# Performance work log

Hardware: AMD Instinct MI355X
Metric: run time of the kernel (lower is better)

Reference implementation:

```python
import jax, jax.numpy as jnp
import numpy as np

N = 100000
F_IN = 256
F_OUT = 64
E = 3200000
NEG_SLOPE = 0.2


def setup_inputs() -> dict:
    key = jax.random.key(0)
    k1, k2, k3, k4, k5 = jax.random.split(key, 5)
    x = jax.random.normal(k1, (N, F_IN), dtype=jnp.float32)
    edge_index = jax.random.randint(k2, (2, E), 0, N, dtype=jnp.int32)
    # GATConv params (heads=1): lin weight, att_src, att_dst, bias
    W = jax.random.normal(k3, (F_IN, F_OUT), dtype=jnp.float32) / np.sqrt(F_IN)
    att_src = jax.random.normal(k4, (F_OUT,), dtype=jnp.float32) / np.sqrt(F_OUT)
    att_dst = jax.random.normal(k5, (F_OUT,), dtype=jnp.float32) / np.sqrt(F_OUT)
    bias = jnp.zeros((F_OUT,), dtype=jnp.float32)
    return {"x": x, "edge_index": edge_index, "W": W,
            "att_src": att_src, "att_dst": att_dst, "bias": bias}


def reference(x, edge_index, W, att_src, att_dst, bias):
    n = x.shape[0]
    h = x @ W  # [N, F_OUT]
    # add self-loops (PyG default add_self_loops=True)
    loops = jnp.arange(n, dtype=edge_index.dtype)
    src = jnp.concatenate([edge_index[0], loops])  # message source j
    dst = jnp.concatenate([edge_index[1], loops])  # message target i
    # per-node attention halves
    a_src = h @ att_src  # [N]
    a_dst = h @ att_dst  # [N]
    e = a_src[src] + a_dst[dst]  # [E+N]
    e = jnp.where(e > 0, e, NEG_SLOPE * e)  # LeakyReLU(0.2)
    # softmax over edges grouped by target node
    e_max = jax.ops.segment_max(e, dst, num_segments=n)
    e_max = jnp.where(jnp.isfinite(e_max), e_max, 0.0)
    p = jnp.exp(e - e_max[dst])
    denom = jax.ops.segment_sum(p, dst, num_segments=n)
    alpha = p / (denom[dst] + 1e-16)  # [E+N]
    # scatter-aggregate weighted source features
    out = jax.ops.segment_sum(alpha[:, None] * h[src], dst, num_segments=n)
    return out + bias
```

## Files before the change

kernel.cpp:

```cpp
#include <hip/hip_runtime.h>
#include <hip/hip_bf16.h>
#include <math.h>

#define F_IN 256
#define F_OUT 64
#define NEG_SLOPE 0.2f
#define SHIFT 7
#define NPB 128
#define MAXK 1024
#define CAP 4608
#define OVF 4
#define GRID_B 256

__device__ __forceinline__ float bf2f(__hip_bfloat16 v) {
    return __bfloat162float(v);
}

typedef short short8 __attribute__((ext_vector_type(8)));
typedef float f32x4 __attribute__((ext_vector_type(4)));

__device__ __forceinline__ unsigned int bf16_bits(float v) {
    unsigned int u = __float_as_uint(v);
    return (u + 0x7fffu + ((u >> 16) & 1u)) >> 16;
}

#define WHI(q, c, l) (((((q)*4 + (c)) * 64) + (l)) * 8)
#define WLO(q, c, l) (16384 + WHI(q, c, l))

__global__ __launch_bounds__(512, 2) void gemm_kernel(
    const float* __restrict__ x, const float* __restrict__ W,
    const float* __restrict__ att_src, const float* __restrict__ att_dst,
    __hip_bfloat16* __restrict__ h16, float* __restrict__ a_src,
    float* __restrict__ a_dst, int N, int nTiles)
{
    __shared__ unsigned short sW[32768];

    const int t = threadIdx.x;
    const int lane = t & 63;
    const int w = t >> 6;
    const int g = lane >> 4;
    const int fr = lane & 15;

    for (int idx = t; idx < 2048; idx += 512) {
        const int q = idx >> 8;
        const int c = (idx >> 6) & 3;
        const int l = idx & 63;
        const int col = c * 16 + (l & 15);
        const float* wp = W + (size_t)(q * 32 + ((l >> 4) * 8)) * F_OUT + col;
        short8 hv, lv;
#pragma unroll
        for (int e = 0; e < 8; e++) {
            float wv = wp[(size_t)e * F_OUT];
            unsigned int hb = bf16_bits(wv);
            float hf = __uint_as_float(hb << 16);
            unsigned int lb = bf16_bits(wv - hf);
            hv[e] = (short)hb;
            lv[e] = (short)lb;
        }
        *(short8*)&sW[WHI(q, c, l)] = hv;
        *(short8*)&sW[WLO(q, c, l)] = lv;
    }
    __syncthreads();

    float as4[4], ad4[4];
#pragma unroll
    for (int c = 0; c < 4; c++) {
        as4[c] = att_src[c * 16 + fr];
        ad4[c] = att_dst[c * 16 + fr];
    }

    const float4 z4 = make_float4(0.f, 0.f, 0.f, 0.f);

    for (int tile = blockIdx.x; tile < nTiles; tile += gridDim.x) {
        const int R0 = tile * 128 + w * 16;
        const int rowA = R0 + fr;
        const bool okA = rowA < N;
        const float* xrow = x + (size_t)rowA * F_IN + g * 8;

        f32x4 acc[4];
#pragma unroll
        for (int c = 0; c < 4; c++) acc[c] = (f32x4){0.f, 0.f, 0.f, 0.f};

        float4 cur0 = okA ? *(const float4*)(xrow + 0) : z4;
        float4 cur1 = okA ? *(const float4*)(xrow + 4) : z4;

#pragma unroll
        for (int q = 0; q < 8; q++) {
            float4 nxt0 = z4, nxt1 = z4;
            if (q < 7) {
                nxt0 = okA ? *(const float4*)(xrow + (q + 1) * 32)     : z4;
                nxt1 = okA ? *(const float4*)(xrow + (q + 1) * 32 + 4) : z4;
            }

            const float vf[8] = {cur0.x, cur0.y, cur0.z, cur0.w,
                                 cur1.x, cur1.y, cur1.z, cur1.w};
            short8 ahi, alo;
#pragma unroll
            for (int e = 0; e < 8; e++) {
                unsigned int hb = bf16_bits(vf[e]);
                float hf = __uint_as_float(hb << 16);
                unsigned int lb = bf16_bits(vf[e] - hf);
                ahi[e] = (short)hb;
                alo[e] = (short)lb;
            }
#pragma unroll
            for (int c = 0; c < 4; c++) {
                short8 bh = *(const short8*)&sW[WHI(q, c, lane)];
                short8 bl = *(const short8*)&sW[WLO(q, c, lane)];
                acc[c] = __builtin_amdgcn_mfma_f32_16x16x32_bf16(ahi, bh, acc[c], 0, 0, 0);
                acc[c] = __builtin_amdgcn_mfma_f32_16x16x32_bf16(alo, bh, acc[c], 0, 0, 0);
                acc[c] = __builtin_amdgcn_mfma_f32_16x16x32_bf16(ahi, bl, acc[c], 0, 0, 0);
            }
            cur0 = nxt0;
            cur1 = nxt1;
            __builtin_amdgcn_sched_barrier(0);
        }

        float sr[4] = {0.f, 0.f, 0.f, 0.f};
        float sd[4] = {0.f, 0.f, 0.f, 0.f};
#pragma unroll
        for (int c = 0; c < 4; c++) {
#pragma unroll
            for (int r = 0; r < 4; r++) {
                float v = acc[c][r];
                sr[r] = fmaf(v, as4[c], sr[r]);
                sd[r] = fmaf(v, ad4[c], sd[r]);
            }
        }
#pragma unroll
        for (int off = 1; off <= 8; off <<= 1) {
#pragma unroll
            for (int r = 0; r < 4; r++) {
                sr[r] += __shfl_xor(sr[r], off, 64);
                sd[r] += __shfl_xor(sd[r], off, 64);
            }
        }

#pragma unroll
        for (int r = 0; r < 4; r++) {
            const int row = R0 + g * 4 + r;
            if (row < N) {
                unsigned int lo = bf16_bits(acc[0][r]) | (bf16_bits(acc[1][r]) << 16);
                unsigned int hi = bf16_bits(acc[2][r]) | (bf16_bits(acc[3][r]) << 16);
                *(int2*)(h16 + (size_t)row * F_OUT + fr * 4) = make_int2((int)lo, (int)hi);
            }
        }

        if (fr < 4) {
            const int row = R0 + g * 4 + fr;
            if (row < N) {
                float vs = (fr == 0) ? sr[0] : (fr == 1) ? sr[1] : (fr == 2) ? sr[2] : sr[3];
                float vd = (fr == 0) ? sd[0] : (fr == 1) ? sd[1] : (fr == 2) ? sd[2] : sd[3];
                a_src[row] = vs;
                a_dst[row] = vd;
            }
        }
    }
}

__global__ __launch_bounds__(1024) void bucket_count_kernel(
    const int* __restrict__ dst, int* __restrict__ pbh, int E, int K, int R)
{
    __shared__ int s[MAXK];
    const int t = threadIdx.x;
    for (int b = t; b < K; b += 1024) s[b] = 0;
    __syncthreads();
    const int start = blockIdx.x * R;
    const int end = min(E, start + R);
    for (int e = start + t * 4; e < end; e += 4096) {
        if (e + 3 < end) {
            int4 d = *(const int4*)&dst[e];
            atomicAdd(&s[d.x >> SHIFT], 1);
            atomicAdd(&s[d.y >> SHIFT], 1);
            atomicAdd(&s[d.z >> SHIFT], 1);
            atomicAdd(&s[d.w >> SHIFT], 1);
        } else {
            for (int q = e; q < end; q++) atomicAdd(&s[dst[q] >> SHIFT], 1);
        }
    }
    __syncthreads();
    int* row = pbh + (size_t)blockIdx.x * K;
    for (int b = t; b < K; b += 1024) row[b] = s[b];
}

__global__ __launch_bounds__(64) void colscan_kernel(
    const int* __restrict__ pbh, int* __restrict__ cbase,
    int* __restrict__ btot, int K, int NBLK)
{
    const int k = blockIdx.x;
    const int lane = threadIdx.x;
    int v[4];
#pragma unroll
    for (int c = 0; c < 4; c++) {
        int b = c * 64 + lane;
        v[c] = (b < NBLK) ? pbh[(size_t)b * K + k] : 0;
    }
    int carry = 0;
#pragma unroll
    for (int c = 0; c < 4; c++) {
        int orig = v[c];
        int s = v[c];
#pragma unroll
        for (int off = 1; off < 64; off <<= 1) {
            int u = __shfl_up(s, off, 64);
            if (lane >= off) s += u;
        }
        int b = c * 64 + lane;
        if (b < NBLK) cbase[(size_t)b * K + k] = carry + s - orig;
        carry += __shfl(s, 63, 64);
    }
    if (lane == 0) btot[k] = carry;
}

__global__ __launch_bounds__(1024) void bbase_scan_kernel(
    const int* __restrict__ btot, int* __restrict__ bbase, int K, int E)
{
    __shared__ int s[1024];
    const int t = threadIdx.x;
    int v = (t < K) ? btot[t] : 0;
    s[t] = v;
    __syncthreads();
    for (int off = 1; off < 1024; off <<= 1) {
        int u = (t >= off) ? s[t - off] : 0;
        __syncthreads();
        s[t] += u;
        __syncthreads();
    }
    if (t < K) bbase[t] = s[t] - v;
    if (t == 0) bbase[K] = E;
}

__global__ __launch_bounds__(1024) void bin_kernel(
    const int* __restrict__ ei, const int* __restrict__ cbase,
    const int* __restrict__ bbase, int* __restrict__ rec, int E, int K, int R)
{
    __shared__ int cb[MAXK];
    const int t = threadIdx.x;
    const int start = blockIdx.x * R;
    const int end = min(E, start + R);
    const int* crow = cbase + (size_t)blockIdx.x * K;
    for (int b = t; b < K; b += 1024) cb[b] = bbase[b] + crow[b];
    __syncthreads();

    for (int e = start + t * 4; e < end; e += 4096) {
        if (e + 3 < end) {
            int4 jj = *(const int4*)&ei[e];
            int4 ii = *(const int4*)&ei[E + e];
            int p0 = atomicAdd(&cb[ii.x >> SHIFT], 1);
            int p1 = atomicAdd(&cb[ii.y >> SHIFT], 1);
            int p2 = atomicAdd(&cb[ii.z >> SHIFT], 1);
            int p3 = atomicAdd(&cb[ii.w >> SHIFT], 1);
            rec[p0] = jj.x | ((ii.x & (NPB - 1)) << 17);
            rec[p1] = jj.y | ((ii.y & (NPB - 1)) << 17);
            rec[p2] = jj.z | ((ii.z & (NPB - 1)) << 17);
            rec[p3] = jj.w | ((ii.w & (NPB - 1)) << 17);
        } else {
            for (int q = e; q < end; q++) {
                int j = ei[q], i = ei[E + q];
                int pos = atomicAdd(&cb[i >> SHIFT], 1);
                rec[pos] = j | ((i & (NPB - 1)) << 17);
            }
        }
    }
}

__global__ __launch_bounds__(256) void sort_kernel(
    int* __restrict__ rec, const int* __restrict__ bbase,
    int* __restrict__ row_ptr, int N, int E, int K)
{
    __shared__ int stage[CAP];
    __shared__ int deg[NPB];
    __shared__ int sval[NPB];
    __shared__ int base[NPB];
    __shared__ int cnt[NPB];
    const int t = threadIdx.x;
    const int b = blockIdx.x;
    const int s = bbase[b], e = bbase[b + 1];
    const int tot = e - s;
    const int nodeBase = b << SHIFT;
    const int nodes = min(NPB, N - nodeBase);

    if (t < NPB) deg[t] = 0;
    __syncthreads();

    int ovf[OVF];
    for (int r = t; r < tot; r += 256) {
        int m = rec[s + r];
        if (r < CAP) stage[r] = m;
        else { int k = (r - CAP) >> 8; if (k < OVF) ovf[k] = m; }
        atomicAdd(&deg[(m >> 17) & (NPB - 1)], 1);
    }
    __syncthreads();

    if (t < NPB) sval[t] = deg[t];
    __syncthreads();
    for (int off = 1; off < NPB; off <<= 1) {
        int v = (t < NPB && t >= off) ? sval[t - off] : 0;
        __syncthreads();
        if (t < NPB) sval[t] += v;
        __syncthreads();
    }
    if (t < NPB) {
        base[t] = sval[t] - deg[t];
        cnt[t] = 0;
        if (t < nodes) row_ptr[nodeBase + t] = s + base[t];
    }
    if (b == K - 1 && t == 0) row_ptr[N] = E;
    __syncthreads();

    for (int r = t; r < tot; r += 256) {
        int m = (r < CAP) ? stage[r] : ovf[(r - CAP) >> 8];
        int li = (m >> 17) & (NPB - 1);
        int rk = atomicAdd(&cnt[li], 1);
        rec[s + base[li] + rk] = m;
    }
}

__global__ __launch_bounds__(256) void node_kernel(
    const __hip_bfloat16* __restrict__ h16, const float* __restrict__ a_src,
    const float* __restrict__ a_dst, const int* __restrict__ row_ptr,
    const int* __restrict__ rec, const float* __restrict__ bias,
    float* __restrict__ out, int N)
{
    const int w = threadIdx.x >> 6;
    const int lane = threadIdx.x & 63;
    const int i = blockIdx.x * 4 + w;
    if (i >= N) return;

    const int pcol = ((lane & 15) << 2) | (lane >> 4);

    const int s = row_ptr[i];
    const int e = row_ptr[i + 1];

    const float adst_i = a_dst[i];
    float vs = a_src[i] + adst_i;
    vs = fmaxf(vs, NEG_SLOPE * vs);
    const float pself = __expf(vs);
    float denl = (lane == 0) ? pself : 0.f;
    float acc = pself * bf2f(h16[(size_t)i * F_OUT + pcol]);

    for (int k = s; k < e; k += 64) {
        const int cnt = min(64, e - k);
        int r = (lane < cnt) ? rec[k + lane] : 0;
        int j = r & 0x1FFFF;
        float v = a_src[j] + adst_i;
        v = fmaxf(v, NEG_SLOPE * v);
        float p = __expf(v);
        if (lane >= cnt) p = 0.f;
        denl += p;

        int u = 0;
        for (; u + 8 <= cnt; u += 8) {
            int ju[8]; float pu[8], g[8];
#pragma unroll
            for (int c = 0; c < 8; c++) {
                ju[c] = __shfl(j, u + c, 64);
                pu[c] = __shfl(p, u + c, 64);
            }
#pragma unroll
            for (int c = 0; c < 8; c++)
                g[c] = bf2f(h16[(size_t)ju[c] * F_OUT + pcol]);
            asm volatile("" ::: "memory");
#pragma unroll
            for (int c = 0; c < 8; c++)
                acc = fmaf(pu[c], g[c], acc);
        }
        for (; u < cnt; u++) {
            int jc = __shfl(j, u, 64);
            float pc = __shfl(p, u, 64);
            acc = fmaf(pc, bf2f(h16[(size_t)jc * F_OUT + pcol]), acc);
        }
    }

    float den = denl;
#pragma unroll
    for (int o = 32; o > 0; o >>= 1) den += __shfl_xor(den, o, 64);

    out[(size_t)i * F_OUT + lane] = acc / (den + 1e-16f) + bias[lane];
}

extern "C" void kernel_launch(void* const* d_in, const int* in_sizes, int n_in,
                              void* d_out, int out_size, void* d_ws, size_t ws_size,
                              hipStream_t stream)
{
    const float* x      = (const float*)d_in[0];
    const int*   ei     = (const int*)d_in[1];
    const float* W      = (const float*)d_in[2];
    const float* att_sr = (const float*)d_in[3];
    const float* att_ds = (const float*)d_in[4];
    const float* bias   = (const float*)d_in[5];
    float* out = (float*)d_out;

    const int N = in_sizes[0] / F_IN;
    const int E = in_sizes[1] / 2;
    const int K = (N + NPB - 1) >> SHIFT;
    const int R = (((E + GRID_B - 1) / GRID_B) + 3) & ~3;

    char* ws = (char*)d_ws;
    size_t off = 0;
    auto alloc = [&](size_t bytes) -> void* {
        void* p = ws + off;
        off = (off + bytes + 255) & ~(size_t)255;
        return p;
    };
    __hip_bfloat16* h16 = (__hip_bfloat16*)alloc((size_t)N * F_OUT * 2);
    float* a_src   = (float*)alloc((size_t)N * 4);
    float* a_dst   = (float*)alloc((size_t)N * 4);
    int*   pbh     = (int*)alloc((size_t)GRID_B * K * 4);
    int*   cbase   = (int*)alloc((size_t)GRID_B * K * 4);
    int*   btot    = (int*)alloc((size_t)K * 4);
    int*   bbase   = (int*)alloc((size_t)(K + 1) * 4);
    int*   row_ptr = (int*)alloc((size_t)(N + 1) * 4);
    int*   rec     = (int*)alloc((size_t)E * 4);
    (void)ws_size; (void)n_in; (void)out_size;

    const int nTiles = (N + 127) >> 7;
    const int gemmGrid = nTiles < 512 ? nTiles : 512;

    gemm_kernel<<<gemmGrid, 512, 0, stream>>>(x, W, att_sr, att_ds, h16, a_src, a_dst, N, nTiles);
    bucket_count_kernel<<<GRID_B, 1024, 0, stream>>>(ei + E, pbh, E, K, R);
    colscan_kernel<<<K, 64, 0, stream>>>(pbh, cbase, btot, K, GRID_B);
    bbase_scan_kernel<<<1, 1024, 0, stream>>>(btot, bbase, K, E);
    bin_kernel<<<GRID_B, 1024, 0, stream>>>(ei, cbase, bbase, rec, E, K, R);
    sort_kernel<<<K, 256, 0, stream>>>(rec, bbase, row_ptr, N, E, K);
    node_kernel<<<(N + 3) / 4, 256, 0, stream>>>(h16, a_src, a_dst, row_ptr, rec, bias, out, N);
}
```

Before: 371.3 us.

## Gather four neighbor rows per load with 8-byte vector reads in node kernel

Reworks the node aggregation so each lane loads 4 packed bf16 values (8 bytes) and 16 lanes cover one neighbor row. A single wave instruction therefore fetches 4 neighbor rows, and all 16 loads for a 64-edge chunk are issued before the exp/weight computation, replacing the per-edge scalar bf16 gather loop. Partial sums are combined with cross-quarter shuffles, and the bf16-to-float conversion is done with bit shifts. The chunk always processes 64 slots (padded slots load row 0 with weight 0), which adds redundant loads for low-degree nodes and more register use for the 16 in-flight int2 values.

```diff
diff --git a/kernel.cpp b/kernel.cpp
--- a/kernel.cpp
+++ b/kernel.cpp
@@ -327,7 +327,9 @@
     const int i = blockIdx.x * 4 + w;
     if (i >= N) return;
 
-    const int pcol = ((lane & 15) << 2) | (lane >> 4);
+    const int q = lane >> 4;
+    const int a = lane & 15;
+    const unsigned short* __restrict__ hb = (const unsigned short*)h16;
 
     const int s = row_ptr[i];
     const int e = row_ptr[i + 1];
@@ -337,46 +339,66 @@
     vs = fmaxf(vs, NEG_SLOPE * vs);
     const float pself = __expf(vs);
     float denl = (lane == 0) ? pself : 0.f;
-    float acc = pself * bf2f(h16[(size_t)i * F_OUT + pcol]);
+
+    float acc0 = 0.f, acc1 = 0.f, acc2 = 0.f, acc3 = 0.f;
 
     for (int k = s; k < e; k += 64) {
         const int cnt = min(64, e - k);
         int r = (lane < cnt) ? rec[k + lane] : 0;
         int j = r & 0x1FFFF;
-        float v = a_src[j] + adst_i;
+
+        float asj = a_src[j];
+
+        int2 d[16];
+#pragma unroll
+        for (int g = 0; g < 16; g++) {
+            int jsel = __shfl(j, 4 * g + q, 64);
+            d[g] = *(const int2*)(hb + (size_t)jsel * F_OUT + a * 4);
+        }
+
+        float v = asj + adst_i;
         v = fmaxf(v, NEG_SLOPE * v);
         float p = __expf(v);
         if (lane >= cnt) p = 0.f;
         denl += p;
 
-        int u = 0;
-        for (; u + 8 <= cnt; u += 8) {
-            int ju[8]; float pu[8], g[8];
-#pragma unroll
-            for (int c = 0; c < 8; c++) {
-                ju[c] = __shfl(j, u + c, 64);
-                pu[c] = __shfl(p, u + c, 64);
-            }
-#pragma unroll
-            for (int c = 0; c < 8; c++)
-                g[c] = bf2f(h16[(size_t)ju[c] * F_OUT + pcol]);
-            asm volatile("" ::: "memory");
-#pragma unroll
-            for (int c = 0; c < 8; c++)
-                acc = fmaf(pu[c], g[c], acc);
-        }
-        for (; u < cnt; u++) {
-            int jc = __shfl(j, u, 64);
-            float pc = __shfl(p, u, 64);
-            acc = fmaf(pc, bf2f(h16[(size_t)jc * F_OUT + pcol]), acc);
-        }
-    }
-
+#pragma unroll
+        for (int g = 0; g < 16; g++) {
+            float psel = __shfl(p, 4 * g + q, 64);
+            unsigned int lo = (unsigned int)d[g].x;
+            unsigned int hi = (unsigned int)d[g].y;
+            acc0 = fmaf(psel, __uint_as_float(lo << 16), acc0);
+            acc1 = fmaf(psel, __uint_as_float(lo & 0xFFFF0000u), acc1);
+            acc2 = fmaf(psel, __uint_as_float(hi << 16), acc2);
+            acc3 = fmaf(psel, __uint_as_float(hi & 0xFFFF0000u), acc3);
+        }
+    }
+
+#pragma unroll
+    for (int o = 16; o <= 32; o <<= 1) {
+        acc0 += __shfl_xor(acc0, o, 64);
+        acc1 += __shfl_xor(acc1, o, 64);
+        acc2 += __shfl_xor(acc2, o, 64);
+        acc3 += __shfl_xor(acc3, o, 64);
+    }
     float den = denl;
 #pragma unroll
     for (int o = 32; o > 0; o >>= 1) den += __shfl_xor(den, o, 64);
-
-    out[(size_t)i * F_OUT + lane] = acc / (den + 1e-16f) + bias[lane];
+    den += 1e-16f;
+
+    if (lane < 16) {
+        int2 hs = *(const int2*)(hb + (size_t)i * F_OUT + a * 4);
+        unsigned int lo = (unsigned int)hs.x, hi = (unsigned int)hs.y;
+        float s0 = acc0 + pself * __uint_as_float(lo << 16);
+        float s1 = acc1 + pself * __uint_as_float(lo & 0xFFFF0000u);
+        float s2 = acc2 + pself * __uint_as_float(hi << 16);
+        float s3 = acc3 + pself * __uint_as_float(hi & 0xFFFF0000u);
+        float* orow = out + (size_t)i * F_OUT;
+        orow[ 0 + a] = s0 / den + bias[ 0 + a];
+        orow[16 + a] = s1 / den + bias[16 + a];
+        orow[32 + a] = s2 / den + bias[32 + a];
+        orow[48 + a] = s3 / den + bias[48 + a];
+    }
 }
 
 extern "C" void kernel_launch(void* const* d_in, const int* in_sizes, int n_in,
```

Result: faster. 331.2 us (-10.8%).

## Gather 16-byte bf16 row chunks per lane, process two nodes per wave

Applied to the files above, without the earlier changes.

Rewrites the aggregation kernel so each lane loads a 16-byte chunk (8 bf16 features) of a neighbor row, and the wave covers 8 neighbors per group instead of one 2-byte element per lane. Each wave now handles two destination nodes and interleaves their edge chunks to expose more independent loads. Neighbor indices and weights are passed through LDS, and the partial sums are combined across the 8 neighbor slots with an LDS reduction. This cuts the number of gather instructions and raises memory-level parallelism, at the cost of more LDS traffic, more registers (16 int4 buffers) and load imbalance when the two nodes have different degrees.

```diff
diff --git a/kernel.cpp b/kernel.cpp
--- a/kernel.cpp
+++ b/kernel.cpp
@@ -322,61 +322,161 @@
     const int* __restrict__ rec, const float* __restrict__ bias,
     float* __restrict__ out, int N)
 {
+    __shared__ int   sj[4][2][64];
+    __shared__ float sp[4][2][64];
+    __shared__ float cmb[4][8][65];
+
     const int w = threadIdx.x >> 6;
     const int lane = threadIdx.x & 63;
-    const int i = blockIdx.x * 4 + w;
-    if (i >= N) return;
-
-    const int pcol = ((lane & 15) << 2) | (lane >> 4);
-
-    const int s = row_ptr[i];
-    const int e = row_ptr[i + 1];
-
-    const float adst_i = a_dst[i];
-    float vs = a_src[i] + adst_i;
-    vs = fmaxf(vs, NEG_SLOPE * vs);
-    const float pself = __expf(vs);
-    float denl = (lane == 0) ? pself : 0.f;
-    float acc = pself * bf2f(h16[(size_t)i * F_OUT + pcol]);
-
-    for (int k = s; k < e; k += 64) {
-        const int cnt = min(64, e - k);
-        int r = (lane < cnt) ? rec[k + lane] : 0;
-        int j = r & 0x1FFFF;
-        float v = a_src[j] + adst_i;
-        v = fmaxf(v, NEG_SLOPE * v);
-        float p = __expf(v);
-        if (lane >= cnt) p = 0.f;
-        denl += p;
-
-        int u = 0;
-        for (; u + 8 <= cnt; u += 8) {
-            int ju[8]; float pu[8], g[8];
-#pragma unroll
-            for (int c = 0; c < 8; c++) {
-                ju[c] = __shfl(j, u + c, 64);
-                pu[c] = __shfl(p, u + c, 64);
-            }
-#pragma unroll
-            for (int c = 0; c < 8; c++)
-                g[c] = bf2f(h16[(size_t)ju[c] * F_OUT + pcol]);
-            asm volatile("" ::: "memory");
-#pragma unroll
-            for (int c = 0; c < 8; c++)
-                acc = fmaf(pu[c], g[c], acc);
-        }
-        for (; u < cnt; u++) {
-            int jc = __shfl(j, u, 64);
-            float pc = __shfl(p, u, 64);
-            acc = fmaf(pc, bf2f(h16[(size_t)jc * F_OUT + pcol]), acc);
-        }
-    }
-
-    float den = denl;
-#pragma unroll
-    for (int o = 32; o > 0; o >>= 1) den += __shfl_xor(den, o, 64);
-
-    out[(size_t)i * F_OUT + lane] = acc / (den + 1e-16f) + bias[lane];
+    const int i0 = blockIdx.x * 8 + w * 2;
+    if (i0 >= N) return;
+    const int i1 = i0 + 1;
+    const bool has1 = (i1 < N);
+
+    const int o  = lane >> 3;
+    const int a8 = lane & 7;
+    const unsigned short* __restrict__ hb = (const unsigned short*)h16;
+    const unsigned short* __restrict__ hba = hb + a8 * 8;
+
+    const int*   sj0 = &sj[w][0][o];
+    const int*   sj1 = &sj[w][1][o];
+    const float* sp0 = &sp[w][0][o];
+    const float* sp1 = &sp[w][1][o];
+
+    const int s0   = row_ptr[i0];
+    const int mid  = row_ptr[i0 + 1];
+    const int e1x  = has1 ? row_ptr[i0 + 2] : mid;
+
+    int kcur0 = s0,  end0 = mid;
+    int kcur1 = mid, end1 = e1x;
+
+    const float adst0 = a_dst[i0];
+    const int   i1c   = has1 ? i1 : i0;
+    const float adst1 = a_dst[i1c];
+    float v0 = a_src[i0] + adst0;  v0 = fmaxf(v0, NEG_SLOPE * v0);
+    float v1 = a_src[i1c] + adst1; v1 = fmaxf(v1, NEG_SLOPE * v1);
+    const float pself0 = __expf(v0);
+    const float pself1 = __expf(v1);
+    float den0 = (lane == 0) ? pself0 : 0.f;
+    float den1 = (lane == 0) ? pself1 : 0.f;
+
+    float4 aL0 = make_float4(0.f,0.f,0.f,0.f), aH0 = aL0;
+    float4 aL1 = aL0, aH1 = aL0;
+
+    while (kcur0 < end0 || kcur1 < end1) {
+        const int cnt0 = (kcur0 < end0) ? min(64, end0 - kcur0) : 0;
+        const int cnt1 = (kcur1 < end1) ? min(64, end1 - kcur1) : 0;
+        const int G0 = (cnt0 + 7) >> 3;
+        const int G1 = (cnt1 + 7) >> 3;
+
+        int r0 = (lane < cnt0) ? rec[kcur0 + lane] : 0;
+        int r1 = (lane < cnt1) ? rec[kcur1 + lane] : 0;
+        int j0 = r0 & 0x1FFFF;
+        int j1 = r1 & 0x1FFFF;
+        sj[w][0][lane] = j0;
+        sj[w][1][lane] = j1;
+        float as0 = a_src[j0];
+        float as1 = a_src[j1];
+        __builtin_amdgcn_sched_barrier(0);
+
+        int4 d0[8], d1[8];
+#pragma unroll
+        for (int g = 0; g < 8; g++) {
+            if (g < G0) {
+                int jsel = sj0[8 * g];
+                d0[g] = *(const int4*)(hba + (size_t)jsel * F_OUT);
+            }
+        }
+#pragma unroll
+        for (int g = 0; g < 8; g++) {
+            if (g < G1) {
+                int jsel = sj1[8 * g];
+                d1[g] = *(const int4*)(hba + (size_t)jsel * F_OUT);
+            }
+        }
+
+        float u0 = as0 + adst0; u0 = fmaxf(u0, NEG_SLOPE * u0);
+        float u1 = as1 + adst1; u1 = fmaxf(u1, NEG_SLOPE * u1);
+        float p0 = __expf(u0);
+        float p1 = __expf(u1);
+        if (lane >= cnt0) p0 = 0.f;
+        if (lane >= cnt1) p1 = 0.f;
+        den0 += p0;
+        den1 += p1;
+        sp[w][0][lane] = p0;
+        sp[w][1][lane] = p1;
+        __builtin_amdgcn_sched_barrier(0);
+
+#pragma unroll
+        for (int g = 0; g < 8; g++) {
+            if (g < G0) {
+                float ps = sp0[8 * g];
+                unsigned int dx = (unsigned int)d0[g].x, dy = (unsigned int)d0[g].y;
+                unsigned int dz = (unsigned int)d0[g].z, dw = (unsigned int)d0[g].w;
+                aL0.x = fmaf(ps, __uint_as_float(dx << 16),          aL0.x);
+                aL0.y = fmaf(ps, __uint_as_float(dx & 0xFFFF0000u),  aL0.y);
+                aL0.z = fmaf(ps, __uint_as_float(dy << 16),          aL0.z);
+                aL0.w = fmaf(ps, __uint_as_float(dy & 0xFFFF0000u),  aL0.w);
+                aH0.x = fmaf(ps, __uint_as_float(dz << 16),          aH0.x);
+                aH0.y = fmaf(ps, __uint_as_float(dz & 0xFFFF0000u),  aH0.y);
+                aH0.z = fmaf(ps, __uint_as_float(dw << 16),          aH0.z);
+                aH0.w = fmaf(ps, __uint_as_float(dw & 0xFFFF0000u),  aH0.w);
+            }
+        }
+#pragma unroll
+        for (int g = 0; g < 8; g++) {
+            if (g < G1) {
+                float ps = sp1[8 * g];
+                unsigned int dx = (unsigned int)d1[g].x, dy = (unsigned int)d1[g].y;
+                unsigned int dz = (unsigned int)d1[g].z, dw = (unsigned int)d1[g].w;
+                aL1.x = fmaf(ps, __uint_as_float(dx << 16),          aL1.x);
+                aL1.y = fmaf(ps, __uint_as_float(dx & 0xFFFF0000u),  aL1.y);
+                aL1.z = fmaf(ps, __uint_as_float(dy << 16),          aL1.z);
+                aL1.w = fmaf(ps, __uint_as_float(dy & 0xFFFF0000u),  aL1.w);
+                aH1.x = fmaf(ps, __uint_as_float(dz << 16),          aH1.x);
+                aH1.y = fmaf(ps, __uint_as_float(dz & 0xFFFF0000u),  aH1.y);
+                aH1.z = fmaf(ps, __uint_as_float(dw << 16),          aH1.z);
+                aH1.w = fmaf(ps, __uint_as_float(dw & 0xFFFF0000u),  aH1.w);
+            }
+        }
+        __builtin_amdgcn_sched_barrier(0);
+
+        if (kcur0 < end0) kcur0 += 64;
+        if (kcur1 < end1) kcur1 += 64;
+    }
+
+#pragma unroll
+    for (int off = 32; off > 0; off >>= 1) {
+        den0 += __shfl_xor(den0, off, 64);
+        den1 += __shfl_xor(den1, off, 64);
+    }
+    den0 += 1e-16f;
+    den1 += 1e-16f;
+
+    const int pl = ((lane & 15) << 2) | (lane >> 4);
+
+    *(float4*)&cmb[w][o][a8 * 8]     = aL0;
+    *(float4*)&cmb[w][o][a8 * 8 + 4] = aH0;
+    __builtin_amdgcn_sched_barrier(0);
+    {
+        float sum = cmb[w][0][pl] + cmb[w][1][pl] + cmb[w][2][pl] + cmb[w][3][pl]
+                  + cmb[w][4][pl] + cmb[w][5][pl] + cmb[w][6][pl] + cmb[w][7][pl];
+        float hself = __uint_as_float((unsigned int)hb[(size_t)i0 * F_OUT + pl] << 16);
+        sum += pself0 * hself;
+        out[(size_t)i0 * F_OUT + lane] = sum / den0 + bias[lane];
+    }
+    __builtin_amdgcn_sched_barrier(0);
+
+    if (has1) {
+        *(float4*)&cmb[w][o][a8 * 8]     = aL1;
+        *(float4*)&cmb[w][o][a8 * 8 + 4] = aH1;
+        __builtin_amdgcn_sched_barrier(0);
+        float sum = cmb[w][0][pl] + cmb[w][1][pl] + cmb[w][2][pl] + cmb[w][3][pl]
+                  + cmb[w][4][pl] + cmb[w][5][pl] + cmb[w][6][pl] + cmb[w][7][pl];
+        float hself = __uint_as_float((unsigned int)hb[(size_t)i1 * F_OUT + pl] << 16);
+        sum += pself1 * hself;
+        out[(size_t)i1 * F_OUT + lane] = sum / den1 + bias[lane];
+    }
 }
 
 extern "C" void kernel_launch(void* const* d_in, const int* in_sizes, int n_in,
@@ -423,5 +523,5 @@
     bbase_scan_kernel<<<1, 1024, 0, stream>>>(btot, bbase, K, E);
     bin_kernel<<<GRID_B, 1024, 0, stream>>>(ei, cbase, bbase, rec, E, K, R);
     sort_kernel<<<K, 256, 0, stream>>>(rec, bbase, row_ptr, N, E, K);
-    node_kernel<<<(N + 3) / 4, 256, 0, stream>>>(h16, a_src, a_dst, row_ptr, rec, bias, out, N);
-}
+    node_kernel<<<(N + 7) / 8, 256, 0, stream>>>(h16, a_src, a_dst, row_ptr, rec, bias, out, N);
+}
```

After: 326.0 us. 12.2% less time.
